# Kernel optimization log

Measured on AMD Instinct MI355X. Metric: run time of the kernel, lower is better.

## Reference

```python
import jax, jax.numpy as jnp
import numpy as np
import math

D_MODEL = 1024
N_HEADS = 16
FACTOR = 5


def setup_inputs() -> dict:
    key = jax.random.key(0)
    ks = jax.random.split(key, 8)
    B, L, S, d = 8, 4096, 4096, D_MODEL
    sc = 1.0 / math.sqrt(d)
    perm = jnp.asarray(np.random.default_rng(0).permutation(L), jnp.int32)
    return {
        "queries": jax.random.normal(ks[0], (B, L, d), jnp.float32),
        "keys": jax.random.normal(ks[1], (B, S, d), jnp.float32),
        "values": jax.random.normal(ks[2], (B, S, d), jnp.float32),
        "perm": perm,
        "Wq": jax.random.normal(ks[3], (d, d), jnp.float32) * sc,
        "bq": jnp.zeros((d,), jnp.float32),
        "Wk": jax.random.normal(ks[4], (d, d), jnp.float32) * sc,
        "bk": jnp.zeros((d,), jnp.float32),
        "Wv": jax.random.normal(ks[5], (d, d), jnp.float32) * sc,
        "bv": jnp.zeros((d,), jnp.float32),
        "Wo": jax.random.normal(ks[6], (d, d), jnp.float32) * sc,
        "bo": jnp.zeros((d,), jnp.float32),
    }


def reference(queries, keys, values, perm, Wq, bq, Wk, bk, Wv, bv, Wo, bo):
    B, L, d = queries.shape
    S = keys.shape[1]
    H = N_HEADS
    dk = d // H

    q = (queries @ Wq + bq).reshape(B, L, H, dk)
    k = (keys @ Wk + bk).reshape(B, S, H, dk)
    v = (values @ Wv + bv).reshape(B, S, H, dk)

    # ProbSparse: u = min(factor * ceil(log(S)), L)  (static, shape-derived)
    u_part = FACTOR * int(math.ceil(math.log(S)))
    u = min(u_part, L)

    # sample u queries (perm replaces torch.randperm for determinism)
    q_sample = q[:, perm[:u]]                                   # [B,u,H,dk]
    scores_sample = jnp.einsum('buhd,bshd->bhus', q_sample, k)  # [B,H,u,S]

    # sparsity measurement M = max_s - mean_s
    M = scores_sample.max(-1) - scores_sample.sum(-1) / S       # [B,H,u]
    _, M_top = jax.lax.top_k(M, u)                              # [B,H,u] indices in [0,u)

    # gather top-u queries per (batch, head) along the L axis
    qT = q.transpose(0, 2, 1, 3)                                # [B,H,L,dk]
    q_red = jnp.take_along_axis(qT, M_top[..., None], axis=2)   # [B,H,u,dk]

    scores = jnp.einsum('bhud,bshd->bhus', q_red, k)            # [B,H,u,S]
    attn = jax.nn.softmax(scores, axis=-1)
    context = jnp.einsum('bhus,bshd->buhd', attn, v).reshape(B, u, d)
    output = context @ Wo + bo                                  # [B,u,d]
    return output, attn
```

## Files before the change

### kernel.cpp

```cpp
#include <hip/hip_runtime.h>
#include <stdint.h>
#include <stddef.h>

#define DEV static __device__ __forceinline__

typedef short short8 __attribute__((ext_vector_type(8)));
typedef short short4v __attribute__((ext_vector_type(4)));
typedef float f32x4 __attribute__((ext_vector_type(4)));
typedef _Float16 half8 __attribute__((ext_vector_type(8)));

DEV uint16_t f2h(float x){
  union { _Float16 h; uint16_t u; } c; c.h = (_Float16)x; return c.u;
}

DEV f32x4 mfma16h(short8 a, short8 b, f32x4 c){
  union { short8 s; half8 h; } ua, ub; ua.s = a; ub.s = b;
  return __builtin_amdgcn_mfma_f32_16x16x32_f16(ua.h, ub.h, c, 0, 0, 0);
}

typedef const __attribute__((address_space(1))) void* gas1;
typedef __attribute__((address_space(3))) void* las3;
DEV void async16(const void* g, void* l){
  __builtin_amdgcn_global_load_lds((gas1)g, (las3)l, 16, 0, 0);
}

DEV int swzoct(int row, int oct){ return (oct & ~7) | ((oct ^ row) & 7); }
DEV short8 lds_frag(const short* base, int row, int rowOcts, int oct){
  int o = swzoct(row, oct);
  return *(const short8*)(base + row * rowOcts * 8 + o * 8);
}
DEV void lds_store8(short* base, int row, int rowOcts, int oct, short8 v){
  int o = swzoct(row, oct);
  *(short8*)(base + row * rowOcts * 8 + o * 8) = v;
}

__global__ __launch_bounds__(256) void pa_prep_weights(
    const float* __restrict__ Wk, const float* __restrict__ Wv,
    uint16_t* WkT, uint16_t* WvT){
  int which = blockIdx.y;
  const float* W = which ? Wv : Wk;
  uint16_t* O = which ? WvT : WkT;
  int e0 = (blockIdx.x * 256 + threadIdx.x) * 4;
  #pragma unroll
  for(int c=0;c<4;c++){
    int e = e0 + c; int n = e >> 10, k = e & 1023;
    O[e] = f2h(W[(size_t)k*1024 + n]);
  }
}

__global__ __launch_bounds__(256) void pa_q_stage1(
    const float* __restrict__ queries, const int* __restrict__ perm,
    const float* __restrict__ Wq, double* __restrict__ qpart){
  __shared__ alignas(16) float Alds[96*32];
  __shared__ alignas(16) float Blds[32*128];
  int ct = blockIdx.x, kc = blockIdx.y, b = blockIdx.z;
  int t = threadIdx.x;
  int tr = t >> 4, tc = t & 15;
  const float* qb = queries + (size_t)b*4096*1024;
  const float* srcA[3];
  #pragma unroll
  for(int rr=0; rr<3; rr++){
    int chunk = rr*256 + t;
    int row = chunk >> 3, c8 = chunk & 7;
    int rid = (row < 45) ? perm[row] : (row < 90 ? row - 45 : 0);
    srcA[rr] = qb + (size_t)rid*1024 + c8*4;
  }
  const float* srcB[4];
  #pragma unroll
  for(int rr=0; rr<4; rr++){
    int chunk = rr*256 + t;
    int kk = chunk >> 5, c = chunk & 31;
    srcB[rr] = Wq + (size_t)kk*1024 + ct*128 + c*4;
  }
  double acc[6][8];
  #pragma unroll
  for(int i=0;i<6;i++)
    #pragma unroll
    for(int jj=0;jj<8;jj++) acc[i][jj] = 0.0;
  int k0 = kc*128;
  for(int ks=0; ks<4; ks++){
    int kk0 = k0 + ks*32;
    #pragma unroll
    for(int rr=0; rr<3; rr++)
      async16(srcA[rr] + kk0, (char*)Alds + (rr*256 + t)*16);
    #pragma unroll
    for(int rr=0; rr<4; rr++)
      async16(srcB[rr] + (size_t)kk0*1024, (char*)Blds + (rr*256 + t)*16);
    __syncthreads();
    #pragma unroll
    for(int kk=0; kk<32; kk++){
      double av[6];
      #pragma unroll
      for(int i=0;i<6;i++) av[i] = (double)Alds[(tr*6+i)*32 + kk];
      float4 b0 = *(const float4*)(Blds + kk*128 + tc*8);
      float4 b1 = *(const float4*)(Blds + kk*128 + tc*8 + 4);
      double bv[8] = {(double)b0.x,(double)b0.y,(double)b0.z,(double)b0.w,
                      (double)b1.x,(double)b1.y,(double)b1.z,(double)b1.w};
      #pragma unroll
      for(int i=0;i<6;i++)
        #pragma unroll
        for(int jj=0;jj<8;jj++)
          acc[i][jj] += av[i]*bv[jj];
    }
    __syncthreads();
  }
  #pragma unroll
  for(int i=0;i<6;i++){
    int r = tr*6 + i;
    double* dst = qpart + (((size_t)b*96 + r)*8 + kc)*1024 + ct*128 + tc*8;
    #pragma unroll
    for(int jj=0;jj<8;jj++) dst[jj] = acc[i][jj];
  }
}

__global__ __launch_bounds__(256) void pa_q_finalize(
    const double* __restrict__ qpart, const float* __restrict__ bq,
    float* q_f32, uint16_t* q_f16){
  int slot = blockIdx.x, b = blockIdx.y;
  int j = (slot < 45) ? slot : ((slot >= 48 && slot < 93) ? (45 + slot - 48) : -1);
  #pragma unroll
  for(int c=0;c<4;c++){
    int n = threadIdx.x * 4 + c;
    float v = 0.f;
    if(j >= 0){
      const double* p = qpart + (((size_t)b*96 + j)*8)*1024 + n;
      double s = 0.0;
      #pragma unroll
      for(int kc=0;kc<8;kc++) s += p[(size_t)kc*1024];
      v = (float)(s + (double)bq[n]);
    }
    int h = n >> 6, d = n & 63;
    size_t idx = (((size_t)(b*16 + h))*96 + slot)*64 + d;
    q_f32[idx] = v;
    q_f16[idx] = f2h(v);
  }
}

__global__ __launch_bounds__(256) void pa_kv_gemm(
    const float* __restrict__ keys, const float* __restrict__ values,
    const uint16_t* __restrict__ WkT, const uint16_t* __restrict__ WvT,
    const float* __restrict__ bk, const float* __restrict__ bv,
    uint16_t* __restrict__ k_o, uint16_t* __restrict__ v_t){
  __shared__ alignas(16) short Ah[128*64], Bh[128*64];
  const bool TR = (blockIdx.y == 1);
  const float* Ag = TR ? values : keys;
  const uint16_t* Bg = TR ? WvT : WkT;
  const float* bias = TR ? bv : bk;
  int tid = threadIdx.x, wid = tid >> 6, lane = tid & 63;
  int bid = blockIdx.x;
  int xcd = bid & 7, slot = bid >> 3;
  int mt = xcd*32 + (slot >> 3), nt = slot & 7;
  int m0 = mt*128, n0 = nt*128;
  int rsub = lane >> 3;
  int soct = (lane & 7) ^ rsub;
  const float*    aF = Ag + (size_t)(m0 + wid*32 + rsub)*1024 + soct*8;
  const uint16_t* b0 = Bg + (size_t)(n0 + wid*32 + rsub)*1024 + soct*8;
  short* lA = Ah + wid*32*64;
  short* lB = Bh + wid*32*64;
  f32x4 acc[4][4];
  #pragma unroll
  for(int i=0;i<4;i++)
    #pragma unroll
    for(int jj=0;jj<4;jj++) acc[i][jj] = (f32x4){0.f,0.f,0.f,0.f};
  int wr = wid >> 1, wc = wid & 1;
  for(int kb=0; kb<16; kb++){
    int ko = kb*64;
    #pragma unroll
    for(int q=0;q<4;q++)
      async16(b0 + ko + q*8*1024, lB + q*512);
    #pragma unroll
    for(int q=0;q<4;q++){
      const float* src = aF + ko + (size_t)q*8*1024;
      float4 u0 = *(const float4*)(src);
      float4 u1 = *(const float4*)(src + 4);
      short8 hv;
      hv[0]=(short)f2h(u0.x); hv[1]=(short)f2h(u0.y);
      hv[2]=(short)f2h(u0.z); hv[3]=(short)f2h(u0.w);
      hv[4]=(short)f2h(u1.x); hv[5]=(short)f2h(u1.y);
      hv[6]=(short)f2h(u1.z); hv[7]=(short)f2h(u1.w);
      *(short8*)(lA + q*512 + lane*8) = hv;
    }
    __syncthreads();
    short8 Af[4][2];
    #pragma unroll
    for(int mf=0;mf<4;mf++)
      #pragma unroll
      for(int k2=0;k2<2;k2++){
        int row = wr*64 + mf*16 + (lane & 15);
        int oct = k2*4 + (lane >> 4);
        Af[mf][k2] = lds_frag(Ah, row, 8, oct);
      }
    #pragma unroll
    for(int nf=0;nf<4;nf++){
      short8 Bf[2];
      #pragma unroll
      for(int k2=0;k2<2;k2++){
        int row = wc*64 + nf*16 + (lane & 15);
        int oct = k2*4 + (lane >> 4);
        Bf[k2] = lds_frag(Bh, row, 8, oct);
      }
      #pragma unroll
      for(int mf=0;mf<4;mf++)
        #pragma unroll
        for(int k2=0;k2<2;k2++)
          acc[mf][nf] = mfma16h(Af[mf][k2], Bf[k2], acc[mf][nf]);
    }
    __syncthreads();
  }
  int b = m0 >> 12, s_base = m0 & 4095;
  #pragma unroll
  for(int mf=0;mf<4;mf++)
    #pragma unroll
    for(int nf=0;nf<4;nf++){
      int srow = s_base + wr*64 + mf*16 + ((lane >> 4) << 2);
      int ncol = n0 + wc*64 + nf*16 + (lane & 15);
      float bia = bias[ncol];
      int h = ncol >> 6, d = ncol & 63;
      if(!TR){
        size_t base = ((((size_t)(b*16 + h))*4096 + srow)*64 + d);
        #pragma unroll
        for(int i=0;i<4;i++)
          k_o[base + (size_t)i*64] = f2h(acc[mf][nf][i] + bia);
      } else {
        short4v pk;
        #pragma unroll
        for(int i=0;i<4;i++) pk[i] = (short)f2h(acc[mf][nf][i] + bia);
        *(short4v*)(v_t + ((((size_t)(b*16 + h))*64 + d)*4096 + srow)) = pk;
      }
    }
}

__global__ __launch_bounds__(256) void pa_p1_stats(
    const uint16_t* __restrict__ q_f16, const uint16_t* __restrict__ khg,
    float* __restrict__ stats){
  __shared__ alignas(16) short qf[96*64], kh[128*64];
  int chunk = blockIdx.x, h = blockIdx.y, b = blockIdx.z;
  int tid = threadIdx.x, wid = tid >> 6, lane = tid & 63;
  const uint16_t* qsf = q_f16 + ((size_t)(b*16 + h))*96*64;
  #pragma unroll
  for(int jj=0;jj<3;jj++){
    int oc = tid*3 + jj;
    int sl = oc >> 3, o = oc & 7;
    lds_store8(qf, sl, 8, o, *(const short8*)(qsf + sl*64 + o*8));
  }
  float t1v[3][4], t2v[3][4], t3v[3][4], ssum[3][4], mm[3][4], zz[3][4];
  int t1i[3][4], t2i[3][4], t3i[3][4];
  #pragma unroll
  for(int a=0;a<3;a++)
    #pragma unroll
    for(int i=0;i<4;i++){
      t1v[a][i]=-3e38f; t2v[a][i]=-3e38f; t3v[a][i]=-3e38f; ssum[a][i]=0.f;
      mm[a][i]=-3e38f; zz[a][i]=0.f; t1i[a][i]=0; t2i[a][i]=0; t3i[a][i]=0;
    }
  int rsub = lane >> 3, soct = (lane & 7) ^ rsub;
  const uint16_t* khb = khg + (((size_t)(b*16 + h))*4096)*64;
  __syncthreads();
  for(int st=0; st<4; st++){
    int sg0 = chunk*512 + st*128;
    #pragma unroll
    for(int q=0;q<4;q++){
      int row = wid*32 + q*8;
      async16(khb + (size_t)(sg0 + row + rsub)*64 + soct*8, kh + row*64);
    }
    __syncthreads();
    short8 Bf[2][2];
    #pragma unroll
    for(int nf=0;nf<2;nf++)
      #pragma unroll
      for(int k2=0;k2<2;k2++){
        int scol = wid*32 + nf*16 + (lane & 15);
        int oct = k2*4 + (lane >> 4);
        Bf[nf][k2] = lds_frag(kh, scol, 8, oct);
      }
    #pragma unroll
    for(int mf=0;mf<6;mf++){
      short8 af[2];
      #pragma unroll
      for(int k2=0;k2<2;k2++){
        int row = mf*16 + (lane & 15);
        int oct = k2*4 + (lane >> 4);
        af[k2] = lds_frag(qf, row, 8, oct);
      }
      f32x4 a0 = (f32x4){0.f,0.f,0.f,0.f}, a1 = a0;
      #pragma unroll
      for(int k2=0;k2<2;k2++){
        a0 = mfma16h(af[k2], Bf[0][k2], a0);
        a1 = mfma16h(af[k2], Bf[1][k2], a1);
      }
      #pragma unroll
      for(int nf=0;nf<2;nf++){
        int sgl = sg0 + wid*32 + nf*16 + (lane & 15);
        #pragma unroll
        for(int i=0;i<4;i++){
          float v = nf ? a1[i] : a0[i];
          if(mf < 3){
            ssum[mf][i] += v;
            if(v > t1v[mf][i]){
              t3v[mf][i]=t2v[mf][i]; t3i[mf][i]=t2i[mf][i];
              t2v[mf][i]=t1v[mf][i]; t2i[mf][i]=t1i[mf][i];
              t1v[mf][i]=v; t1i[mf][i]=sgl;
            } else if(v > t2v[mf][i]){
              t3v[mf][i]=t2v[mf][i]; t3i[mf][i]=t2i[mf][i];
              t2v[mf][i]=v; t2i[mf][i]=sgl;
            } else if(v > t3v[mf][i]){
              t3v[mf][i]=v; t3i[mf][i]=sgl;
            }
          } else {
            int q = mf - 3;
            float mn = fmaxf(mm[q][i], v);
            zz[q][i] = zz[q][i]*__expf(mm[q][i]-mn) + __expf(v-mn);
            mm[q][i] = mn;
          }
        }
      }
    }
    __syncthreads();
  }
  size_t sbase = (((((size_t)b*16 + h)*8 + chunk)*4 + wid)*96)*8;
  #pragma unroll
  for(int mf=0;mf<3;mf++)
    #pragma unroll
    for(int i=0;i<4;i++){
      float v1=t1v[mf][i], v2=t2v[mf][i], v3=t3v[mf][i], sm=ssum[mf][i];
      int i1=t1i[mf][i], i2=t2i[mf][i], i3=t3i[mf][i];
      #pragma unroll
      for(int msk=1; msk<16; msk<<=1){
        float w1=__shfl_xor(v1,msk,64), w2=__shfl_xor(v2,msk,64), w3=__shfl_xor(v3,msk,64);
        int j1=__shfl_xor(i1,msk,64), j2=__shfl_xor(i2,msk,64), j3=__shfl_xor(i3,msk,64);
        sm += __shfl_xor(sm,msk,64);
        if(w1 > v1){
          float tv; int ti;
          tv=v1; v1=w1; w1=tv; ti=i1; i1=j1; j1=ti;
          tv=v2; v2=w2; w2=tv; ti=i2; i2=j2; j2=ti;
          tv=v3; v3=w3; w3=tv; ti=i3; i3=j3; j3=ti;
        }
        if(w1 > v2){
          v3=v2; i3=i2; v2=w1; i2=j1;
          if(w2 > v3){ v3=w2; i3=j2; }
        } else if(w1 > v3){ v3=w1; i3=j1; }
      }
      if((lane & 15) == 0){
        int sl = mf*16 + ((lane >> 4) << 2) + i;
        float* dst = stats + sbase + (size_t)sl*8;
        dst[0]=v1; dst[1]=__int_as_float(i1); dst[2]=v2; dst[3]=__int_as_float(i2);
        dst[4]=v3; dst[5]=__int_as_float(i3); dst[6]=sm;
      }
    }
  #pragma unroll
  for(int q=0;q<3;q++)
    #pragma unroll
    for(int i=0;i<4;i++){
      float m1=mm[q][i], z1=zz[q][i];
      #pragma unroll
      for(int msk=1; msk<16; msk<<=1){
        float m2=__shfl_xor(m1,msk,64), z2=__shfl_xor(z1,msk,64);
        float mn = fmaxf(m1,m2);
        z1 = z1*__expf(m1-mn) + z2*__expf(m2-mn);
        m1 = mn;
      }
      if((lane & 15) == 0){
        int sl = 48 + q*16 + ((lane >> 4) << 2) + i;
        float* dst = stats + sbase + (size_t)sl*8;
        dst[0]=m1; dst[1]=z1;
      }
    }
}

__global__ __launch_bounds__(256) void pa_sort_mark(
    const float* __restrict__ stats,
    float* __restrict__ mzfin,
    float* __restrict__ Mv_g, float* __restrict__ Ssum_g,
    int* __restrict__ mlist_g, int* __restrict__ clist_g,
    int* __restrict__ nmark_g){
  int h = blockIdx.x, b = blockIdx.y;
  int bh = b*16 + h;
  __shared__ float Mv[48], Ssum[48];
  __shared__ int I1[48], I2[48], I3[48];
  __shared__ int order[48], mlist[48], flags[48];
  __shared__ int clist[144];
  __shared__ int nmark;
  int t = threadIdx.x;
  const float* sb = stats + (((size_t)bh)*8*4*96)*8;
  if(t < 48) flags[t] = 0;
  if(t < 48){
    float v1=-3e38f, v2=-3e38f, v3=-3e38f, sm=0.f; int i1=0, i2=0, i3=0;
    for(int c=0;c<8;c++)
      for(int w=0;w<4;w++){
        const float* p = sb + (((size_t)c*4 + w)*96 + t)*8;
        float w1=p[0], w2=p[2], w3=p[4];
        int j1=__float_as_int(p[1]), j2=__float_as_int(p[3]), j3=__float_as_int(p[5]);
        sm += p[6];
        if(w1 > v1){
          float tv; int ti;
          tv=v1; v1=w1; w1=tv; ti=i1; i1=j1; j1=ti;
          tv=v2; v2=w2; w2=tv; ti=i2; i2=j2; j2=ti;
          tv=v3; v3=w3; w3=tv; ti=i3; i3=j3; j3=ti;
        }
        if(w1 > v2){
          v3=v2; i3=i2; v2=w1; i2=j1;
          if(w2 > v3){ v3=w2; i3=j2; }
        } else if(w1 > v3){ v3=w1; i3=j1; }
      }
    Mv[t] = v1 - sm*(1.0f/4096.0f);
    I1[t]=i1; I2[t]=i2; I3[t]=i3; Ssum[t]=sm;
  }
  if(t >= 64 && t < 112){
    int i = t - 64;
    float m1=-3e38f, z1=0.f;
    for(int c=0;c<8;c++)
      for(int w=0;w<4;w++){
        const float* p = sb + (((size_t)c*4 + w)*96 + 48 + i)*8;
        float m2=p[0], z2=p[1];
        float mn = fmaxf(m1,m2);
        z1 = z1*__expf(m1-mn) + z2*__expf(m2-mn);
        m1 = mn;
      }
    mzfin[((size_t)bh*48 + i)*2 + 0] = m1;
    mzfin[((size_t)bh*48 + i)*2 + 1] = z1;
  }
  __syncthreads();
  if(t < 64){
    float v = (t < 45) ? Mv[t] : -3e38f;
    int rank = 0;
    #pragma unroll
    for(int j=0;j<45;j++){
      float vj = __shfl(v, j, 64);
      rank += (vj > v) || (vj == v && j < (int)t);
    }
    if(t < 45) order[rank] = t;
  }
  __syncthreads();
  if(t < 44){
    if(Mv[order[t]] - Mv[order[t+1]] < 0.025f){
      flags[order[t]] = 1; flags[order[t+1]] = 1;
    }
  }
  __syncthreads();
  if(t == 0){
    int cnt=0;
    for(int i=0;i<45;i++) if(flags[i]){
      clist[3*cnt]   = I1[i];
      clist[3*cnt+1] = I2[i];
      clist[3*cnt+2] = I3[i];
      mlist[cnt++]=i;
    }
    nmark = cnt;
  }
  __syncthreads();
  int nm = nmark;
  if(t < 48){
    Mv_g[(size_t)bh*48 + t] = Mv[t];
    Ssum_g[(size_t)bh*48 + t] = Ssum[t];
  }
  if(t < nm) mlist_g[(size_t)bh*48 + t] = mlist[t];
  if(t < 3*nm) clist_g[(size_t)bh*144 + t] = clist[t];
  if(t == 0) nmark_g[bh] = nm;
}

__global__ __launch_bounds__(256) void pa_refine(
    const float* __restrict__ keys, const float* __restrict__ Wk,
    const float* __restrict__ q_f32,
    const int* __restrict__ mlist_g, const int* __restrict__ clist_g,
    const int* __restrict__ nmark_g, double* __restrict__ scx_g){
  int cid = blockIdx.x, h = blockIdx.y, b = blockIdx.z;
  int bh = b*16 + h;
  int nc = nmark_g[bh]*3;
  if(cid >= nc) return;
  __shared__ double red[256];
  int t = threadIdx.x;
  int kq = t >> 6, d = t & 63;
  int sidx = clist_g[(size_t)bh*144 + cid];
  int u = mlist_g[(size_t)bh*48 + cid/3];
  const float* krow = keys + ((size_t)b*4096 + sidx)*1024;
  double acc = 0.0;
  int col = h*64 + d;
  #pragma unroll 8
  for(int k=kq*256; k<kq*256+256; k++)
    acc += (double)krow[k] * (double)Wk[(size_t)k*1024 + col];
  red[t] = acc;
  __syncthreads();
  if(t < 64){
    double kd = red[t] + red[64+t] + red[128+t] + red[192+t];
    double sp = kd * (double)q_f32[((size_t)bh*96 + u)*64 + t];
    #pragma unroll
    for(int m=1; m<64; m<<=1) sp += __shfl_xor(sp, m, 64);
    if(t == 0) scx_g[(size_t)bh*144 + cid] = sp;
  }
}

__global__ __launch_bounds__(64) void pa_final_rank(
    const float* __restrict__ Mv_g, const float* __restrict__ Ssum_g,
    const int* __restrict__ mlist_g, const int* __restrict__ nmark_g,
    const double* __restrict__ scx_g, int* __restrict__ invrk){
  int h = blockIdx.x, b = blockIdx.y;
  int bh = b*16 + h;
  __shared__ float Mv[48];
  int t = threadIdx.x;
  if(t < 48) Mv[t] = Mv_g[(size_t)bh*48 + t];
  int nm = nmark_g[bh];
  __syncthreads();
  if(t < nm){
    int u = mlist_g[(size_t)bh*48 + t];
    const double* s3 = scx_g + (size_t)bh*144 + 3*t;
    double mx = s3[0];
    if(s3[1] > mx) mx = s3[1];
    if(s3[2] > mx) mx = s3[2];
    Mv[u] = (float)mx - Ssum_g[(size_t)bh*48 + u]*(1.0f/4096.0f);
  }
  __syncthreads();
  float v = (t < 45) ? Mv[t] : -3e38f;
  int rank = 0;
  #pragma unroll
  for(int j=0;j<45;j++){
    float vj = __shfl(v, j, 64);
    rank += (vj > v) || (vj == v && j < (int)t);
  }
  if(t < 45) invrk[(size_t)bh*48 + t] = rank;
}

__global__ __launch_bounds__(256) void pa_p2_attn(
    const uint16_t* __restrict__ q_f16, const uint16_t* __restrict__ khg,
    const uint16_t* __restrict__ v_t,
    const float* __restrict__ mzfin, const int* __restrict__ invrk,
    float* __restrict__ attn_out, float* __restrict__ ctx2){
  __shared__ alignas(16) short qf[48*64];
  __shared__ alignas(16) short kh[64*64];
  __shared__ alignas(16) short vT[64*64];
  __shared__ alignas(16) short Pl[48*64];
  int chunk = blockIdx.x, h = blockIdx.y, b = blockIdx.z;
  int tid = threadIdx.x, wid = tid >> 6, lane = tid & 63;
  const uint16_t* qsf = q_f16 + (((size_t)(b*16 + h))*96 + 48)*64;
  for(int oc=tid; oc<384; oc+=256){
    int sl = oc >> 3, o = oc & 7;
    lds_store8(qf, sl, 8, o, *(const short8*)(qsf + sl*64 + o*8));
  }
  float mreg[3][4], invz[3][4];
  int rrk[3][4];
  #pragma unroll
  for(int mf=0;mf<3;mf++)
    #pragma unroll
    for(int i=0;i<4;i++){
      int u = mf*16 + ((lane >> 4) << 2) + i;
      mreg[mf][i] = mzfin[(((size_t)(b*16 + h))*48 + u)*2 + 0];
      invz[mf][i] = 1.f / mzfin[(((size_t)(b*16 + h))*48 + u)*2 + 1];
      rrk[mf][i] = invrk[((size_t)(b*16 + h))*48 + u];
    }
  f32x4 ctx[3];
  #pragma unroll
  for(int mf=0;mf<3;mf++) ctx[mf] = (f32x4){0.f,0.f,0.f,0.f};
  int rsub = lane >> 3, soct = (lane & 7) ^ rsub;
  const uint16_t* khb = khg + (((size_t)(b*16 + h))*4096)*64;
  const uint16_t* vtb = v_t + (((size_t)(b*16 + h))*64)*4096;
  __syncthreads();
  for(int st=0; st<8; st++){
    int sg0 = chunk*512 + st*64;
    #pragma unroll
    for(int q=0;q<2;q++){
      int row = wid*16 + q*8;
      async16(khb + (size_t)(sg0 + row + rsub)*64 + soct*8, kh + row*64);
      async16(vtb + (size_t)(row + rsub)*4096 + sg0 + soct*8, vT + row*64);
    }
    __syncthreads();
    short8 Bf[2];
    #pragma unroll
    for(int k2=0;k2<2;k2++){
      int scol = wid*16 + (lane & 15);
      int oct = k2*4 + (lane >> 4);
      Bf[k2] = lds_frag(kh, scol, 8, oct);
    }
    #pragma unroll
    for(int mf=0;mf<3;mf++){
      short8 af[2];
      #pragma unroll
      for(int k2=0;k2<2;k2++){
        int row = mf*16 + (lane & 15);
        int oct = k2*4 + (lane >> 4);
        af[k2] = lds_frag(qf, row, 8, oct);
      }
      f32x4 a0 = (f32x4){0.f,0.f,0.f,0.f};
      #pragma unroll
      for(int k2=0;k2<2;k2++)
        a0 = mfma16h(af[k2], Bf[k2], a0);
      int scl = wid*16 + (lane & 15);
      #pragma unroll
      for(int i=0;i<4;i++){
        int u = mf*16 + ((lane >> 4) << 2) + i;
        float p = __expf(a0[i] - mreg[mf][i]) * invz[mf][i];
        if(u < 45){
          attn_out[(((size_t)(b*16 + h))*45 + rrk[mf][i])*4096 + sg0 + scl] = p;
        }
        int oct = scl >> 3;
        int o = (oct ^ (u & 7)) & 7;
        Pl[u*64 + o*8 + (scl & 7)] = (short)f2h(p);
      }
    }
    __syncthreads();
    #pragma unroll
    for(int k2=0;k2<2;k2++){
      int oct = k2*4 + (lane >> 4);
      int drow = wid*16 + (lane & 15);
      short8 bv = lds_frag(vT, drow, 8, oct);
      #pragma unroll
      for(int mf=0;mf<3;mf++){
        int row = mf*16 + (lane & 15);
        short8 ap = lds_frag(Pl, row, 8, oct);
        ctx[mf] = mfma16h(ap, bv, ctx[mf]);
      }
    }
    __syncthreads();
  }
  #pragma unroll
  for(int mf=0;mf<3;mf++)
    #pragma unroll
    for(int i=0;i<4;i++){
      int u = mf*16 + ((lane >> 4) << 2) + i;
      if(u < 45){
        int d = wid*16 + (lane & 15);
        ctx2[(((size_t)chunk*8 + b)*45 + rrk[mf][i])*1024 + h*64 + d] = ctx[mf][i];
      }
    }
}

__global__ __launch_bounds__(256) void pa_out_part(
    const float* __restrict__ ctx2, const float* __restrict__ Wo,
    float* __restrict__ opart){
  __shared__ float cl[8][256];
  int bx = blockIdx.x, by = blockIdx.y, kc = blockIdx.z;
  int t = threadIdx.x;
  for(int e=t; e<8*256; e+=256){
    int rr = e >> 8, kk = e & 255;
    size_t grow = (size_t)by*8 + rr;
    float s = 0.f;
    #pragma unroll
    for(int c=0;c<8;c++) s += ctx2[((size_t)c*360 + grow)*1024 + kc*256 + kk];
    cl[rr][kk] = s;
  }
  __syncthreads();
  int quad = t & 63, rg = t >> 6;
  int n = bx*256 + quad*4;
  float acc[2][4];
  #pragma unroll
  for(int rr=0;rr<2;rr++)
    #pragma unroll
    for(int c=0;c<4;c++) acc[rr][c]=0.f;
  for(int k=0;k<256;k++){
    float4 w = *(const float4*)(Wo + (size_t)(kc*256 + k)*1024 + n);
    float c0 = cl[rg*2][k], c1 = cl[rg*2+1][k];
    acc[0][0] += c0*w.x; acc[0][1] += c0*w.y; acc[0][2] += c0*w.z; acc[0][3] += c0*w.w;
    acc[1][0] += c1*w.x; acc[1][1] += c1*w.y; acc[1][2] += c1*w.z; acc[1][3] += c1*w.w;
  }
  #pragma unroll
  for(int rr=0;rr<2;rr++){
    size_t grow = (size_t)by*8 + rg*2 + rr;
    #pragma unroll
    for(int c=0;c<4;c++)
      opart[((size_t)kc*360 + grow)*1024 + n + c] = acc[rr][c];
  }
}

__global__ __launch_bounds__(256) void pa_out_reduce(
    const float* __restrict__ opart, const float* __restrict__ bo,
    float* __restrict__ out){
  size_t e = (size_t)blockIdx.x*256 + threadIdx.x;
  const size_t N = (size_t)360*1024;
  if(e >= N) return;
  float s = ((opart[e] + opart[e + N]) + opart[e + 2*N]) + opart[e + 3*N];
  out[e] = s + bo[e & 1023];
}

extern "C" void kernel_launch(void* const* d_in, const int* in_sizes, int n_in,
                              void* d_out, int out_size, void* d_ws, size_t ws_size,
                              hipStream_t stream){
  const float* queries = (const float*)d_in[0];
  const float* keys    = (const float*)d_in[1];
  const float* values  = (const float*)d_in[2];
  const int*   perm    = (const int*)d_in[3];
  const float* Wq = (const float*)d_in[4]; const float* bq = (const float*)d_in[5];
  const float* Wk = (const float*)d_in[6]; const float* bk = (const float*)d_in[7];
  const float* Wv = (const float*)d_in[8]; const float* bv = (const float*)d_in[9];
  const float* Wo = (const float*)d_in[10]; const float* bo = (const float*)d_in[11];

  char* ws = (char*)d_ws;
  const size_t SZ = (size_t)33554432;
  uint16_t* k_o   = (uint16_t*)(ws + SZ*4);
  uint16_t* v_t   = (uint16_t*)(ws + SZ*6);
  uint16_t* WkT   = (uint16_t*)(ws + SZ*8);
  uint16_t* WvT   = (uint16_t*)(ws + SZ*8 + 2097152);
  float*    q_f32 = (float*)   (ws + SZ*8 + 4194304);
  uint16_t* q_f16 = (uint16_t*)(ws + SZ*8 + 7340032);

  char* rg = ws + SZ*2;
  double* qpart   = (double*)rg;
  float*  stats   = (float*)rg;
  float*  mzfin   = (float*)(rg + 12582912);
  int*    invrk   = (int*)  (rg + 12632064);
  float*  ctx2    = (float*)(rg + 12656640);
  float*  Mv_g    = (float*)(rg + 24453120);
  float*  Ssum_g  = (float*)(rg + 24477696);
  int*    mlist_g = (int*)  (rg + 24502272);
  int*    clist_g = (int*)  (rg + 24526848);
  int*    nmark_g = (int*)  (rg + 24600576);
  double* scx_g   = (double*)(rg + 24601088);
  float*  opart   = (float*)(rg + 24748544);

  float* out  = (float*)d_out;
  float* attn = out + (size_t)360*1024;

  pa_prep_weights<<<dim3(1024,2), 256, 0, stream>>>(Wk, Wv, WkT, WvT);
  pa_q_stage1<<<dim3(8,8,8), 256, 0, stream>>>(queries, perm, Wq, qpart);
  pa_q_finalize<<<dim3(96,8), 256, 0, stream>>>(qpart, bq, q_f32, q_f16);
  pa_kv_gemm<<<dim3(2048,2), 256, 0, stream>>>(keys, values, WkT, WvT, bk, bv, k_o, v_t);
  pa_p1_stats<<<dim3(8,16,8), 256, 0, stream>>>(q_f16, k_o, stats);
  pa_sort_mark<<<dim3(16,8), 256, 0, stream>>>(stats, mzfin, Mv_g, Ssum_g, mlist_g, clist_g, nmark_g);
  pa_refine<<<dim3(135,16,8), 256, 0, stream>>>(keys, Wk, q_f32, mlist_g, clist_g, nmark_g, scx_g);
  pa_final_rank<<<dim3(16,8), 64, 0, stream>>>(Mv_g, Ssum_g, mlist_g, nmark_g, scx_g, invrk);
  pa_p2_attn<<<dim3(8,16,8), 256, 0, stream>>>(q_f16, k_o, v_t, mzfin, invrk, attn, ctx2);
  pa_out_part<<<dim3(4,45,4), 256, 0, stream>>>(ctx2, Wo, opart);
  pa_out_reduce<<<1440, 256, 0, stream>>>(opart, bo, out);
}
```

Baseline: 563.5 us.

## Double-buffer K/V projection GEMM tiles with register prefetch of next A tile

The K/V projection GEMM now double-buffers the B (weight) tile in LDS and prefetches the next fp32 A tile into registers while the current tile is being multiplied. This aims to overlap global-load latency with MFMA work instead of stalling at the start of each k-iteration. In exchange it uses more LDS and more VGPRs, which may reduce occupancy. Correctness depends on the async LDS load of the next B buffer completing before its sync point, which the trailing barrier appears to cover.

```diff
diff --git a/kernel.cpp b/kernel.cpp
--- a/kernel.cpp
+++ b/kernel.cpp
@@ -141,7 +141,8 @@
     const uint16_t* __restrict__ WkT, const uint16_t* __restrict__ WvT,
     const float* __restrict__ bk, const float* __restrict__ bv,
     uint16_t* __restrict__ k_o, uint16_t* __restrict__ v_t){
-  __shared__ alignas(16) short Ah[128*64], Bh[128*64];
+  __shared__ alignas(16) short Ah[128*64];
+  __shared__ alignas(16) short Bh[2][128*64];
   const bool TR = (blockIdx.y == 1);
   const float* Ag = TR ? values : keys;
   const uint16_t* Bg = TR ? WvT : WkT;
@@ -156,31 +157,47 @@
   const float*    aF = Ag + (size_t)(m0 + wid*32 + rsub)*1024 + soct*8;
   const uint16_t* b0 = Bg + (size_t)(n0 + wid*32 + rsub)*1024 + soct*8;
   short* lA = Ah + wid*32*64;
-  short* lB = Bh + wid*32*64;
   f32x4 acc[4][4];
   #pragma unroll
   for(int i=0;i<4;i++)
     #pragma unroll
     for(int jj=0;jj<4;jj++) acc[i][jj] = (f32x4){0.f,0.f,0.f,0.f};
   int wr = wid >> 1, wc = wid & 1;
+  float4 a_lo[4], a_hi[4];
+  #pragma unroll
+  for(int q=0;q<4;q++)
+    async16(b0 + (size_t)q*8*1024, Bh[0] + wid*32*64 + q*512);
+  #pragma unroll
+  for(int q=0;q<4;q++){
+    const float* src = aF + (size_t)q*8*1024;
+    a_lo[q] = *(const float4*)(src);
+    a_hi[q] = *(const float4*)(src + 4);
+  }
   for(int kb=0; kb<16; kb++){
-    int ko = kb*64;
-    #pragma unroll
-    for(int q=0;q<4;q++)
-      async16(b0 + ko + q*8*1024, lB + q*512);
+    int cur = kb & 1;
     #pragma unroll
     for(int q=0;q<4;q++){
-      const float* src = aF + ko + (size_t)q*8*1024;
-      float4 u0 = *(const float4*)(src);
-      float4 u1 = *(const float4*)(src + 4);
       short8 hv;
-      hv[0]=(short)f2h(u0.x); hv[1]=(short)f2h(u0.y);
-      hv[2]=(short)f2h(u0.z); hv[3]=(short)f2h(u0.w);
-      hv[4]=(short)f2h(u1.x); hv[5]=(short)f2h(u1.y);
-      hv[6]=(short)f2h(u1.z); hv[7]=(short)f2h(u1.w);
+      hv[0]=(short)f2h(a_lo[q].x); hv[1]=(short)f2h(a_lo[q].y);
+      hv[2]=(short)f2h(a_lo[q].z); hv[3]=(short)f2h(a_lo[q].w);
+      hv[4]=(short)f2h(a_hi[q].x); hv[5]=(short)f2h(a_hi[q].y);
+      hv[6]=(short)f2h(a_hi[q].z); hv[7]=(short)f2h(a_hi[q].w);
       *(short8*)(lA + q*512 + lane*8) = hv;
     }
     __syncthreads();
+    if(kb < 15){
+      int ko = (kb+1)*64;
+      #pragma unroll
+      for(int q=0;q<4;q++)
+        async16(b0 + ko + (size_t)q*8*1024, Bh[cur^1] + wid*32*64 + q*512);
+      #pragma unroll
+      for(int q=0;q<4;q++){
+        const float* src = aF + ko + (size_t)q*8*1024;
+        a_lo[q] = *(const float4*)(src);
+        a_hi[q] = *(const float4*)(src + 4);
+      }
+    }
+    const short* Bbase = Bh[cur];
     short8 Af[4][2];
     #pragma unroll
     for(int mf=0;mf<4;mf++)
@@ -197,7 +214,7 @@
       for(int k2=0;k2<2;k2++){
         int row = wc*64 + nf*16 + (lane & 15);
         int oct = k2*4 + (lane >> 4);
-        Bf[k2] = lds_frag(Bh, row, 8, oct);
+        Bf[k2] = lds_frag(Bbase, row, 8, oct);
       }
       #pragma unroll
       for(int mf=0;mf<4;mf++)
```

Result: slower. 692.1 us (+22.8%).
